# Optimization experiments

Measured on AMD Instinct MI355X. Metric: run time of the kernel, lower is better.

## Reference

```python
import jax, jax.numpy as jnp
import numpy as np

IDIM = 128
ODIM = 128
G = 8          # deformable groups
KH = KW = 3
K = KH * KW


def conv3x3(x, w, b):
    # x: [B,C,H,W], w: [O,I,3,3], stride 1, pad 1
    y = jax.lax.conv_general_dilated(x, w, (1, 1), ((1, 1), (1, 1)),
                                     dimension_numbers=('NCHW', 'OIHW', 'NCHW'))
    return y + b[None, :, None, None]


def deform_conv_v2(x, offset, mask, w, b):
    # x: [B,C,H,W]; offset: [B,2*G*K,H,W]; mask: [B,G*K,H,W] (pre-sigmoid)
    B, C, H, W = x.shape
    Cg = C // G
    off = offset.reshape(B, G, 2 * K, H, W)
    dy = off[:, :, 0::2]            # [B,G,K,H,W]
    dx = off[:, :, 1::2]
    m = jax.nn.sigmoid(mask).reshape(B, G, K, H, W)

    ky, kx = jnp.meshgrid(jnp.arange(KH), jnp.arange(KW), indexing='ij')
    ky = ky.reshape(K).astype(x.dtype)
    kx = kx.reshape(K).astype(x.dtype)
    hh = jnp.arange(H, dtype=x.dtype)
    ww = jnp.arange(W, dtype=x.dtype)
    # sampling positions (stride 1, pad 1, dilation 1)
    py = dy + (ky[:, None, None] + hh[None, :, None] - 1.0)   # [B,G,K,H,W]
    px = dx + (kx[:, None, None] + ww[None, None, :] - 1.0)

    y0 = jnp.floor(py)
    x0 = jnp.floor(px)
    ly = py - y0
    lx = px - x0

    x_flat = x.reshape(B, G, Cg, H * W)

    def gather(yi, xi):
        valid = ((yi >= 0) & (yi < H) & (xi >= 0) & (xi < W)).astype(x.dtype)
        yc = jnp.clip(yi, 0, H - 1).astype(jnp.int32)
        xc = jnp.clip(xi, 0, W - 1).astype(jnp.int32)
        idx = (yc * W + xc).reshape(B, G, 1, K * H * W)
        v = jnp.take_along_axis(x_flat, jnp.broadcast_to(idx, (B, G, Cg, K * H * W)), axis=3)
        return v.reshape(B, G, Cg, K, H, W) * valid[:, :, None]

    # bilinear interpolation with zero padding, fused with modulation mask
    v = (gather(y0, x0) * ((1 - ly) * (1 - lx))[:, :, None]
         + gather(y0, x0 + 1) * ((1 - ly) * lx)[:, :, None]
         + gather(y0 + 1, x0) * (ly * (1 - lx))[:, :, None]
         + gather(y0 + 1, x0 + 1) * (ly * lx)[:, :, None])
    v = v * m[:, :, None]                                      # [B,G,Cg,K,H,W]

    wr = w.reshape(w.shape[0], G, Cg, K)
    out = jnp.einsum('bgckhw,ogck->bohw', v, wr)
    return out + b[None, :, None, None]


def setup_inputs() -> dict:
    key = jax.random.key(0)
    ks = jax.random.split(key, 12)
    B, H, W = 2, 96, 96
    s = 0.05
    return {
        'R1': jax.random.normal(ks[0], (B, IDIM, H, W), jnp.float32),
        'Q0': jax.random.normal(ks[1], (B, IDIM, H, W), jnp.float32),
        'w1': jax.random.normal(ks[2], (ODIM, IDIM, 3, 3), jnp.float32) * s,
        'b1': jax.random.normal(ks[3], (ODIM,), jnp.float32) * s,
        'w2': jax.random.normal(ks[4], (ODIM, ODIM, 3, 3), jnp.float32) * s,
        'b2': jax.random.normal(ks[5], (ODIM,), jnp.float32) * s,
        'w_om': jax.random.normal(ks[6], (G * 3 * K, ODIM, 3, 3), jnp.float32) * s,
        'b_om': jax.random.normal(ks[7], (G * 3 * K,), jnp.float32) * s,
        'w_dcn': jax.random.normal(ks[8], (ODIM, IDIM, 3, 3), jnp.float32) * s,
        'b_dcn': jax.random.normal(ks[9], (ODIM,), jnp.float32) * s,
        'w_rq': jax.random.normal(ks[10], (ODIM, 2 * ODIM, 3, 3), jnp.float32) * s,
        'b_rq': jax.random.normal(ks[11], (ODIM,), jnp.float32) * s,
    }


def reference(R1, Q0, w1, b1, w2, b2, w_om, b_om, w_dcn, b_dcn, w_rq, b_rq):
    off = jax.nn.relu(conv3x3(R1 - Q0, w1, b1))
    off = jax.nn.relu(conv3x3(off, w2, b2))
    om = conv3x3(off, w_om, b_om)                 # [B, 3*G*K, H, W]
    o1, o2, mask = jnp.split(om, 3, axis=1)
    offset = jnp.concatenate([o1, o2], axis=1)    # [B, 2*G*K, H, W]
    fea = jax.nn.relu(deform_conv_v2(R1, offset, mask, w_dcn, b_dcn))
    fused = jnp.concatenate([fea, Q0], axis=1)
    return jax.nn.relu(conv3x3(fused, w_rq, b_rq))
```

## Files before the change

### kernel.cpp

```cpp
#include <hip/hip_runtime.h>

#define HH 96
#define WW 96
#define HW 9216
#define NPIX 18432
#define OMC 216
#define PP 9604

typedef __attribute__((ext_vector_type(8))) short short8x;
typedef __attribute__((ext_vector_type(8))) unsigned short ushort8x;
typedef __attribute__((ext_vector_type(4))) float f32x4;

__device__ __forceinline__ f32x4 mfma16(short8x a, short8x b, f32x4 c) {
    return __builtin_amdgcn_mfma_f32_16x16x32_bf16(a, b, c, 0, 0, 0);
}
__device__ __forceinline__ unsigned short f2bf(float f) {
    unsigned int u = __float_as_uint(f);
    u = (u + 0x7FFFu + ((u >> 16) & 1u)) >> 16;
    return (unsigned short)u;
}
__device__ __forceinline__ float bf2f(unsigned short b) {
    return __uint_as_float((unsigned int)b << 16);
}
__device__ __forceinline__ void split2(float v, unsigned short& h, unsigned short& l) {
    h = f2bf(v);
    l = f2bf(v - bf2f(h));
}
__device__ __forceinline__ void gld_lds16(const unsigned short* src, unsigned short* dst) {
    __builtin_amdgcn_global_load_lds(
        (const __attribute__((address_space(1))) unsigned int*)src,
        (__attribute__((address_space(3))) unsigned int*)dst, 16, 0, 0);
}

__global__ __launch_bounds__(256) void zero_borders(
    unsigned short* __restrict__ diffb,
    unsigned short* __restrict__ t1,
    unsigned short* __restrict__ catb)
{
    int i = blockIdx.x * 256 + threadIdx.x;
    if (i >= 776) return;
    int b = i / 388, r = i % 388;
    int y, x;
    if      (r < 98)  { y = 0;          x = r; }
    else if (r < 196) { y = 97;         x = r - 98; }
    else if (r < 292) { y = r - 196 + 1; x = 0; }
    else              { y = r - 292 + 1; x = 97; }
    size_t P = (size_t)b * PP + (size_t)y * 98 + x;
    ushort8x z = {};
    #pragma unroll
    for (int c = 0; c < 32; ++c) *(ushort8x*)&diffb[P * 256 + c * 8] = z;
    #pragma unroll
    for (int c = 0; c < 32; ++c) *(ushort8x*)&t1[P * 256 + c * 8] = z;
    #pragma unroll
    for (int c = 0; c < 64; ++c) *(ushort8x*)&catb[P * 512 + c * 8] = z;
}

__global__ __launch_bounds__(256) void prep_acts(
    const float* __restrict__ R1, const float* __restrict__ Q0,
    float* __restrict__ r1f,
    unsigned short* __restrict__ diffb,
    unsigned short* __restrict__ cat)
{
    __shared__ float tR[128][64];
    __shared__ float tQ[128][64];
    int tid = threadIdx.x;
    int p0  = blockIdx.x * 64;
    int b   = p0 / HW;
    int rem0 = p0 % HW;

    for (int e = tid; e < 2048; e += 256) {
        int c = e >> 4, j = e & 15;
        size_t base = ((size_t)(b * 128 + c)) * HW + rem0;
        *(float4*)&tR[c][j * 4] = *(const float4*)(R1 + base + j * 4);
        *(float4*)&tQ[c][j * 4] = *(const float4*)(Q0 + base + j * 4);
    }
    __syncthreads();

    int p = tid & 63, half = tid >> 6;
    int c0 = half * 32;
    int pix = p0 + p;
    int rm = pix % HW, yy = rm / 96, xx = rm % 96;
    size_t P = (size_t)b * PP + (size_t)(yy + 1) * 98 + xx + 1;
    float rv[32];
    ushort8x dh[4], dl[4], qh[4], ql[4];
    #pragma unroll
    for (int cc = 0; cc < 32; ++cc) {
        float r = tR[c0 + cc][p], q = tQ[c0 + cc][p];
        rv[cc] = r;
        unsigned short h, l;
        split2(r - q, h, l); dh[cc >> 3][cc & 7] = h; dl[cc >> 3][cc & 7] = l;
        split2(q, h, l);     qh[cc >> 3][cc & 7] = h; ql[cc >> 3][cc & 7] = l;
    }
    #pragma unroll
    for (int i = 0; i < 8; ++i)
        *(float4*)&r1f[(size_t)pix * 128 + c0 + i * 4] = *(float4*)&rv[i * 4];
    #pragma unroll
    for (int i = 0; i < 4; ++i) {
        *(ushort8x*)&diffb[P * 256 +       c0 + i * 8] = dh[i];
        *(ushort8x*)&diffb[P * 256 + 128 + c0 + i * 8] = dl[i];
        *(ushort8x*)&cat [P * 512 + 128 + c0 + i * 8] = qh[i];
        *(ushort8x*)&cat [P * 512 + 384 + c0 + i * 8] = ql[i];
    }
}

__global__ __launch_bounds__(256) void prep_w(
    const float* __restrict__ w1, const float* __restrict__ w2,
    const float* __restrict__ wom, const float* __restrict__ bom,
    const float* __restrict__ wrq, const float* __restrict__ wdcn,
    unsigned short* __restrict__ p1, unsigned short* __restrict__ p2,
    unsigned short* __restrict__ pom, unsigned short* __restrict__ prq,
    unsigned short* __restrict__ pdcn, float* __restrict__ bomp)
{
    int idx = blockIdx.x * 256 + threadIdx.x;
    unsigned short h, l;
    if (idx < 147456) {
        int t = idx / 16384, o = (idx >> 7) & 127, ci = idx & 127;
        int src = (o * 128 + ci) * 9 + t;
        split2(w1[src], h, l);  p1[idx] = h;  p1[idx + 147456] = l;
        split2(w2[src], h, l);  p2[idx] = h;  p2[idx + 147456] = l;
        int dd = o * 1152 + t * 128 + ci;
        split2(wdcn[src], h, l); pdcn[dd] = h; pdcn[dd + 147456] = l;
    }
    if (idx < 294912) {
        {
            int t = idx / 32768, o = (idx >> 7) & 255, ci = idx & 127;
            float v = (o < OMC) ? wom[(o * 128 + ci) * 9 + t] : 0.f;
            split2(v, h, l); pom[idx] = h; pom[idx + 294912] = l;
        }
        {
            int t = idx / 32768, o = (idx >> 8) & 127, ci = idx & 255;
            split2(wrq[(o * 256 + ci) * 9 + t], h, l);
            prq[idx] = h; prq[idx + 294912] = l;
        }
    }
    if (idx < 256) bomp[idx] = (idx < OMC) ? bom[idx] : 0.f;
}

template<int CIN, int COUTP, int MODE, bool RELU>
__global__ __launch_bounds__(256, 2) void conv_mfma(
    const unsigned short* __restrict__ in,
    const unsigned short* __restrict__ wpk,
    const float* __restrict__ bias,
    void* __restrict__ outv)
{
    constexpr int NKC = CIN / 32;
    constexpr int NSTEP = 9 * NKC;
    const size_t WPLANE = (size_t)9 * COUTP * CIN;

    __shared__ __align__(16) unsigned short s_buf[2][3072 + 8192];

    int tid = threadIdx.x;
    int wid = tid >> 6, lane = tid & 63;
    int r = lane & 15, q = lane >> 4;
    int bid = blockIdx.x;
    int swz = (bid & 7) * 48 + (bid >> 3);
    int rowid = swz >> 1, half = swz & 1;
    int b = rowid / 96, y = rowid % 96;
    int x0 = half * 48;
    int nbase = blockIdx.y * 128;

    auto stage = [&](int buf, int step) {
        int t = step / NKC, kc = step - t * NKC;
        int dy = t / 3 - 1, dx = t % 3 - 1;
        unsigned short* sb = &s_buf[buf][0];
        {
            int j = tid;
            int m = j >> 7, pl = (j >> 6) & 1, L = j & 63;
            int px = m * 16 + (L & 15), qd = L >> 4;
            const unsigned short* src = in +
                ((size_t)b * PP + (size_t)(y + 1 + dy) * 98 + (x0 + 1 + dx + px)) * (2 * CIN)
                + pl * CIN + kc * 32 + qd * 8;
            gld_lds16(src, sb + (size_t)(wid * 64) * 8);
        }
        if (tid < 128) {
            int j = 256 + tid;
            int m = j >> 7, pl = (j >> 6) & 1, L = j & 63;
            int px = m * 16 + (L & 15), qd = L >> 4;
            const unsigned short* src = in +
                ((size_t)b * PP + (size_t)(y + 1 + dy) * 98 + (x0 + 1 + dx + px)) * (2 * CIN)
                + pl * CIN + kc * 32 + qd * 8;
            gld_lds16(src, sb + (size_t)(256 + wid * 64) * 8);
        }
        const unsigned short* wbase = wpk + ((size_t)t * COUTP + nbase) * CIN + kc * 32;
        #pragma unroll
        for (int c = 0; c < 4; ++c) {
            int j = c * 256 + tid;
            int ni = (j >> 7) & 1, pl = (j >> 6) & 1, L = j & 63;
            int rr = L & 15, qq = L >> 4;
            const unsigned short* src = wbase + (size_t)pl * WPLANE
                + (size_t)(c * 32 + ni * 16 + rr) * CIN + qq * 8;
            gld_lds16(src, sb + 3072 + (size_t)(c * 256 + wid * 64) * 8);
        }
    };

    f32x4 acc[3][2] = {};

    auto compute = [&](int buf) {
        const unsigned short* sb = &s_buf[buf][0];
        short8x AH[3], AL[3], BH[2], BL[2];
        #pragma unroll
        for (int m = 0; m < 3; ++m) {
            AH[m] = *(const short8x*)(sb + m * 1024 + lane * 8);
            AL[m] = *(const short8x*)(sb + m * 1024 + 512 + lane * 8);
        }
        #pragma unroll
        for (int n = 0; n < 2; ++n) {
            BH[n] = *(const short8x*)(sb + 3072 + wid * 2048 + n * 1024 + lane * 8);
            BL[n] = *(const short8x*)(sb + 3072 + wid * 2048 + n * 1024 + 512 + lane * 8);
        }
        #pragma unroll
        for (int m = 0; m < 3; ++m) {
            #pragma unroll
            for (int n = 0; n < 2; ++n) {
                acc[m][n] = mfma16(AH[m], BH[n], acc[m][n]);
                acc[m][n] = mfma16(AL[m], BH[n], acc[m][n]);
                acc[m][n] = mfma16(AH[m], BL[n], acc[m][n]);
            }
        }
    };

    stage(0, 0);
    __syncthreads();
    int cur = 0;
    for (int k = 0; k < NSTEP; ++k) {
        if (k + 1 < NSTEP) stage(cur ^ 1, k + 1);
        compute(cur);
        __syncthreads();
        cur ^= 1;
    }

    #pragma unroll
    for (int m = 0; m < 3; ++m) {
        #pragma unroll
        for (int n = 0; n < 2; ++n) {
            int o = nbase + wid * 32 + n * 16 + r;
            float bv = bias[o];
            #pragma unroll
            for (int j = 0; j < 4; ++j) {
                int px = m * 16 + q * 4 + j;
                int xx = x0 + px;
                float v = acc[m][n][j] + bv;
                if (RELU) v = fmaxf(v, 0.f);
                if (MODE == 0) {
                    size_t P = (size_t)b * PP + (size_t)(y + 1) * 98 + xx + 1;
                    unsigned short h, l; split2(v, h, l);
                    ((unsigned short*)outv)[P * 2 * COUTP + o] = h;
                    ((unsigned short*)outv)[P * 2 * COUTP + COUTP + o] = l;
                } else if (MODE == 1) {
                    if (o < OMC)
                        ((unsigned short*)outv)[((size_t)b * HW + y * 96 + xx) * OMC + o] = f2bf(v);
                } else {
                    ((float*)outv)[((size_t)b * 128 + o) * HW + y * 96 + xx] = v;
                }
            }
        }
    }
}

__global__ __launch_bounds__(256) void deform_mfma(
    const float* __restrict__ xf,
    const unsigned short* __restrict__ omf,
    const unsigned short* __restrict__ wpk,
    const float* __restrict__ bias,
    unsigned short* __restrict__ cat)
{
    __shared__ __align__(16) unsigned short s_vh[16][1152];
    __shared__ __align__(16) unsigned short s_vl[16][1152];

    int tid = threadIdx.x;
    int pix0 = blockIdx.x * 16;
    int b = pix0 / HW;

    for (int e = tid; e < 1152; e += 256) {
        int p = e / 72, gk = e % 72;
        int pix = pix0 + p;
        int rem = pix % HW;
        int hh = rem / 96, ww = rem % 96;
        int g = gk / 9, k = gk % 9;
        const unsigned short* op = omf + (size_t)pix * OMC;
        float dy = bf2f(op[g * 18 + 2 * k]);
        float dx = bf2f(op[g * 18 + 2 * k + 1]);
        float mr = bf2f(op[144 + g * 9 + k]);
        float m = 1.f / (1.f + __expf(-mr));
        float py = dy + (float)(k / 3) + (float)hh - 1.f;
        float px = dx + (float)(k % 3) + (float)ww - 1.f;
        float fy = floorf(py), fx = floorf(px);
        int y0 = (int)fy, x0 = (int)fx;
        float ly = py - fy, lx = px - fx;
        float cw[4] = {(1.f - ly) * (1.f - lx), (1.f - ly) * lx,
                       ly * (1.f - lx), ly * lx};
        const float* cp[4];
        #pragma unroll
        for (int j = 0; j < 4; ++j) {
            int yy = y0 + (j >> 1), xx = x0 + (j & 1);
            bool valid = (yy >= 0) && (yy < HH) && (xx >= 0) && (xx < WW);
            int yc = yy < 0 ? 0 : (yy > 95 ? 95 : yy);
            int xc = xx < 0 ? 0 : (xx > 95 ? 95 : xx);
            cp[j] = xf + ((size_t)(b * HW + yc * 96 + xc)) * 128 + g * 16;
            cw[j] = valid ? cw[j] * m : 0.f;
        }
        int swz = (p & 7) << 3;
        int i0 = k * 128 + g * 16;
        ushort8x vh[2], vl[2];
        #pragma unroll
        for (int cq = 0; cq < 4; ++cq) {
            float4 v0 = *(const float4*)(cp[0] + cq * 4);
            float4 v1 = *(const float4*)(cp[1] + cq * 4);
            float4 v2 = *(const float4*)(cp[2] + cq * 4);
            float4 v3 = *(const float4*)(cp[3] + cq * 4);
            float vv[4] = {
                cw[0]*v0.x + cw[1]*v1.x + cw[2]*v2.x + cw[3]*v3.x,
                cw[0]*v0.y + cw[1]*v1.y + cw[2]*v2.y + cw[3]*v3.y,
                cw[0]*v0.z + cw[1]*v1.z + cw[2]*v2.z + cw[3]*v3.z,
                cw[0]*v0.w + cw[1]*v1.w + cw[2]*v2.w + cw[3]*v3.w};
            #pragma unroll
            for (int cc = 0; cc < 4; ++cc) {
                unsigned short h, l;
                split2(vv[cc], h, l);
                int ei = cq * 4 + cc;
                vh[ei >> 3][ei & 7] = h;
                vl[ei >> 3][ei & 7] = l;
            }
        }
        *(ushort8x*)&s_vh[p][(i0    ) ^ swz] = vh[0];
        *(ushort8x*)&s_vh[p][(i0 + 8) ^ swz] = vh[1];
        *(ushort8x*)&s_vl[p][(i0    ) ^ swz] = vl[0];
        *(ushort8x*)&s_vl[p][(i0 + 8) ^ swz] = vl[1];
    }
    __syncthreads();

    int wid = tid >> 6, lane = tid & 63;
    int r = lane & 15, q = lane >> 4;
    int n0 = wid * 32;
    f32x4 acc0 = {}, acc1 = {};
    const unsigned short* wb = wpk + (size_t)(n0 + r) * 1152 + q * 8;
    int swz = (r & 7) << 3;
    #pragma unroll
    for (int ch = 0; ch < 9; ++ch) {
        short8x ah[4], al[4], b0h[4], b1h[4], b0l[4], b1l[4];
        #pragma unroll
        for (int k2 = 0; k2 < 4; ++k2) {
            const int kc = ch * 4 + k2;
            int e0 = (kc * 32 + q * 8) ^ swz;
            ah[k2]  = *(const short8x*)&s_vh[r][e0];
            al[k2]  = *(const short8x*)&s_vl[r][e0];
            b0h[k2] = *(const short8x*)(wb + kc * 32);
            b1h[k2] = *(const short8x*)(wb + (size_t)16 * 1152 + kc * 32);
            b0l[k2] = *(const short8x*)(wb + 147456 + kc * 32);
            b1l[k2] = *(const short8x*)(wb + 147456 + (size_t)16 * 1152 + kc * 32);
        }
        #pragma unroll
        for (int k2 = 0; k2 < 4; ++k2) {
            acc0 = mfma16(ah[k2], b0h[k2], acc0);
            acc1 = mfma16(ah[k2], b1h[k2], acc1);
            acc0 = mfma16(al[k2], b0h[k2], acc0);
            acc1 = mfma16(al[k2], b1h[k2], acc1);
            acc0 = mfma16(ah[k2], b0l[k2], acc0);
            acc1 = mfma16(ah[k2], b1l[k2], acc1);
        }
    }
    #pragma unroll
    for (int ni = 0; ni < 2; ++ni) {
        f32x4 A = ni ? acc1 : acc0;
        int o = n0 + ni * 16 + r;
        float bv = bias[o];
        #pragma unroll
        for (int j = 0; j < 4; ++j) {
            int pixel = pix0 + q * 4 + j;
            int bb = pixel / HW, rm = pixel % HW;
            int yy = rm / 96, xx = rm % 96;
            size_t P = (size_t)bb * PP + (size_t)(yy + 1) * 98 + xx + 1;
            float v = fmaxf(A[j] + bv, 0.f);
            unsigned short h, l;
            split2(v, h, l);
            cat[P * 512 + o] = h;
            cat[P * 512 + 256 + o] = l;
        }
    }
}

extern "C" void kernel_launch(void* const* d_in, const int* in_sizes, int n_in,
                              void* d_out, int out_size, void* d_ws, size_t ws_size,
                              hipStream_t stream) {
    const float* R1    = (const float*)d_in[0];
    const float* Q0    = (const float*)d_in[1];
    const float* w1    = (const float*)d_in[2];
    const float* b1    = (const float*)d_in[3];
    const float* w2    = (const float*)d_in[4];
    const float* b2    = (const float*)d_in[5];
    const float* w_om  = (const float*)d_in[6];
    const float* b_om  = (const float*)d_in[7];
    const float* w_dcn = (const float*)d_in[8];
    const float* b_dcn = (const float*)d_in[9];
    const float* w_rq  = (const float*)d_in[10];
    const float* b_rq  = (const float*)d_in[11];
    float* outp = (float*)d_out;

    char* w = (char*)d_ws;
    float*          r1f   = (float*)w;          w += (size_t)NPIX * 128 * 4;
    unsigned short* diffb = (unsigned short*)w; w += (size_t)2 * PP * 256 * 2;
    unsigned short* t1    = (unsigned short*)w; w += (size_t)2 * PP * 256 * 2;
    unsigned short* catb  = (unsigned short*)w; w += (size_t)2 * PP * 512 * 2;
    unsigned short* p1    = (unsigned short*)w; w += 2 * 147456 * 2;
    unsigned short* p2    = (unsigned short*)w; w += 2 * 147456 * 2;
    unsigned short* pdcn  = (unsigned short*)w; w += 2 * 147456 * 2;
    unsigned short* pom   = (unsigned short*)w; w += 2 * 294912 * 2;
    unsigned short* prq   = (unsigned short*)w; w += 2 * 294912 * 2;
    float*          bomp  = (float*)w;          w += 256 * 4;
    unsigned short* t2    = diffb;
    unsigned short* omf   = t1;

    zero_borders<<<4, 256, 0, stream>>>(diffb, t1, catb);
    prep_acts<<<288, 256, 0, stream>>>(R1, Q0, r1f, diffb, catb);
    prep_w<<<1152, 256, 0, stream>>>(w1, w2, w_om, b_om, w_rq, w_dcn,
                                     p1, p2, pom, prq, pdcn, bomp);

    conv_mfma<128, 128, 0, true ><<<dim3(384, 1), 256, 0, stream>>>(diffb, p1, b1, t1);
    conv_mfma<128, 128, 0, true ><<<dim3(384, 1), 256, 0, stream>>>(t1,    p2, b2, t2);
    conv_mfma<128, 256, 1, false><<<dim3(384, 2), 256, 0, stream>>>(t2,   pom, bomp, omf);

    deform_mfma<<<1152, 256, 0, stream>>>(r1f, omf, pdcn, b_dcn, catb);

    conv_mfma<256, 128, 2, true ><<<dim3(384, 1), 256, 0, stream>>>(catb, prq, b_rq, outp);
}
```

Baseline: 432.4 us.

## Gather deformable samples from bf16 input and drop low-part split in deform GEMM

R1 is now stored as single bf16 instead of fp32 for the deformable gather, which halves the gather traffic. Sampled values are written to shared memory as one bf16 array rather than a hi/lo split, so the deform GEMM does 4 MFMAs per k-chunk instead of 6. The DCN weight packing is reordered to match a (group, tap, channel) column order so the shared-memory tile can be written contiguously without a swizzle, and launch bounds now request 4 blocks per CU. The cost is lower precision in the deformable-conv input and activations, with possible LDS bank conflicts now that the swizzle is gone.

```diff
diff --git a/kernel.cpp b/kernel.cpp
--- a/kernel.cpp
+++ b/kernel.cpp
@@ -57,7 +57,7 @@
 
 __global__ __launch_bounds__(256) void prep_acts(
     const float* __restrict__ R1, const float* __restrict__ Q0,
-    float* __restrict__ r1f,
+    unsigned short* __restrict__ r1b,
     unsigned short* __restrict__ diffb,
     unsigned short* __restrict__ cat)
 {
@@ -81,21 +81,18 @@
     int pix = p0 + p;
     int rm = pix % HW, yy = rm / 96, xx = rm % 96;
     size_t P = (size_t)b * PP + (size_t)(yy + 1) * 98 + xx + 1;
-    float rv[32];
-    ushort8x dh[4], dl[4], qh[4], ql[4];
+    ushort8x rb[4], dh[4], dl[4], qh[4], ql[4];
     #pragma unroll
     for (int cc = 0; cc < 32; ++cc) {
         float r = tR[c0 + cc][p], q = tQ[c0 + cc][p];
-        rv[cc] = r;
+        rb[cc >> 3][cc & 7] = f2bf(r);
         unsigned short h, l;
         split2(r - q, h, l); dh[cc >> 3][cc & 7] = h; dl[cc >> 3][cc & 7] = l;
         split2(q, h, l);     qh[cc >> 3][cc & 7] = h; ql[cc >> 3][cc & 7] = l;
     }
     #pragma unroll
-    for (int i = 0; i < 8; ++i)
-        *(float4*)&r1f[(size_t)pix * 128 + c0 + i * 4] = *(float4*)&rv[i * 4];
-    #pragma unroll
     for (int i = 0; i < 4; ++i) {
+        *(ushort8x*)&r1b[(size_t)pix * 128 + c0 + i * 8] = rb[i];
         *(ushort8x*)&diffb[P * 256 +       c0 + i * 8] = dh[i];
         *(ushort8x*)&diffb[P * 256 + 128 + c0 + i * 8] = dl[i];
         *(ushort8x*)&cat [P * 512 + 128 + c0 + i * 8] = qh[i];
@@ -118,7 +115,7 @@
         int src = (o * 128 + ci) * 9 + t;
         split2(w1[src], h, l);  p1[idx] = h;  p1[idx + 147456] = l;
         split2(w2[src], h, l);  p2[idx] = h;  p2[idx + 147456] = l;
-        int dd = o * 1152 + t * 128 + ci;
+        int dd = o * 1152 + ((ci >> 4) * 9 + t) * 16 + (ci & 15);
         split2(wdcn[src], h, l); pdcn[dd] = h; pdcn[dd + 147456] = l;
     }
     if (idx < 294912) {
@@ -257,22 +254,21 @@
     }
 }
 
-__global__ __launch_bounds__(256) void deform_mfma(
-    const float* __restrict__ xf,
+__global__ __launch_bounds__(256, 4) void deform_mfma(
+    const unsigned short* __restrict__ xb,
     const unsigned short* __restrict__ omf,
     const unsigned short* __restrict__ wpk,
     const float* __restrict__ bias,
     unsigned short* __restrict__ cat)
 {
-    __shared__ __align__(16) unsigned short s_vh[16][1152];
-    __shared__ __align__(16) unsigned short s_vl[16][1152];
+    __shared__ __align__(16) unsigned short s_v[16][1160];
 
     int tid = threadIdx.x;
     int pix0 = blockIdx.x * 16;
     int b = pix0 / HW;
 
     for (int e = tid; e < 1152; e += 256) {
-        int p = e / 72, gk = e % 72;
+        int p = e & 15, gk = e >> 4;
         int pix = pix0 + p;
         int rem = pix % HW;
         int hh = rem / 96, ww = rem % 96;
@@ -289,43 +285,31 @@
         float ly = py - fy, lx = px - fx;
         float cw[4] = {(1.f - ly) * (1.f - lx), (1.f - ly) * lx,
                        ly * (1.f - lx), ly * lx};
-        const float* cp[4];
+        ushort8x cv0[4], cv1[4];
         #pragma unroll
         for (int j = 0; j < 4; ++j) {
             int yy = y0 + (j >> 1), xx = x0 + (j & 1);
             bool valid = (yy >= 0) && (yy < HH) && (xx >= 0) && (xx < WW);
             int yc = yy < 0 ? 0 : (yy > 95 ? 95 : yy);
             int xc = xx < 0 ? 0 : (xx > 95 ? 95 : xx);
-            cp[j] = xf + ((size_t)(b * HW + yc * 96 + xc)) * 128 + g * 16;
+            const unsigned short* cp =
+                xb + ((size_t)(b * HW + yc * 96 + xc)) * 128 + g * 16;
+            cv0[j] = *(const ushort8x*)cp;
+            cv1[j] = *(const ushort8x*)(cp + 8);
             cw[j] = valid ? cw[j] * m : 0.f;
         }
-        int swz = (p & 7) << 3;
-        int i0 = k * 128 + g * 16;
-        ushort8x vh[2], vl[2];
-        #pragma unroll
-        for (int cq = 0; cq < 4; ++cq) {
-            float4 v0 = *(const float4*)(cp[0] + cq * 4);
-            float4 v1 = *(const float4*)(cp[1] + cq * 4);
-            float4 v2 = *(const float4*)(cp[2] + cq * 4);
-            float4 v3 = *(const float4*)(cp[3] + cq * 4);
-            float vv[4] = {
-                cw[0]*v0.x + cw[1]*v1.x + cw[2]*v2.x + cw[3]*v3.x,
-                cw[0]*v0.y + cw[1]*v1.y + cw[2]*v2.y + cw[3]*v3.y,
-                cw[0]*v0.z + cw[1]*v1.z + cw[2]*v2.z + cw[3]*v3.z,
-                cw[0]*v0.w + cw[1]*v1.w + cw[2]*v2.w + cw[3]*v3.w};
-            #pragma unroll
-            for (int cc = 0; cc < 4; ++cc) {
-                unsigned short h, l;
-                split2(vv[cc], h, l);
-                int ei = cq * 4 + cc;
-                vh[ei >> 3][ei & 7] = h;
-                vl[ei >> 3][ei & 7] = l;
-            }
-        }
-        *(ushort8x*)&s_vh[p][(i0    ) ^ swz] = vh[0];
-        *(ushort8x*)&s_vh[p][(i0 + 8) ^ swz] = vh[1];
-        *(ushort8x*)&s_vl[p][(i0    ) ^ swz] = vl[0];
-        *(ushort8x*)&s_vl[p][(i0 + 8) ^ swz] = vl[1];
+        ushort8x o0, o1;
+        #pragma unroll
+        for (int i = 0; i < 8; ++i) {
+            float v0 = cw[0] * bf2f(cv0[0][i]) + cw[1] * bf2f(cv0[1][i])
+                     + cw[2] * bf2f(cv0[2][i]) + cw[3] * bf2f(cv0[3][i]);
+            float v1 = cw[0] * bf2f(cv1[0][i]) + cw[1] * bf2f(cv1[1][i])
+                     + cw[2] * bf2f(cv1[2][i]) + cw[3] * bf2f(cv1[3][i]);
+            o0[i] = f2bf(v0);
+            o1[i] = f2bf(v1);
+        }
+        *(ushort8x*)&s_v[p][gk * 16    ] = o0;
+        *(ushort8x*)&s_v[p][gk * 16 + 8] = o1;
     }
     __syncthreads();
 
@@ -334,30 +318,27 @@
     int n0 = wid * 32;
     f32x4 acc0 = {}, acc1 = {};
     const unsigned short* wb = wpk + (size_t)(n0 + r) * 1152 + q * 8;
-    int swz = (r & 7) << 3;
-    #pragma unroll
-    for (int ch = 0; ch < 9; ++ch) {
-        short8x ah[4], al[4], b0h[4], b1h[4], b0l[4], b1l[4];
-        #pragma unroll
-        for (int k2 = 0; k2 < 4; ++k2) {
-            const int kc = ch * 4 + k2;
-            int e0 = (kc * 32 + q * 8) ^ swz;
-            ah[k2]  = *(const short8x*)&s_vh[r][e0];
-            al[k2]  = *(const short8x*)&s_vl[r][e0];
-            b0h[k2] = *(const short8x*)(wb + kc * 32);
-            b1h[k2] = *(const short8x*)(wb + (size_t)16 * 1152 + kc * 32);
-            b0l[k2] = *(const short8x*)(wb + 147456 + kc * 32);
-            b1l[k2] = *(const short8x*)(wb + 147456 + (size_t)16 * 1152 + kc * 32);
-        }
-        #pragma unroll
-        for (int k2 = 0; k2 < 4; ++k2) {
-            acc0 = mfma16(ah[k2], b0h[k2], acc0);
-            acc1 = mfma16(ah[k2], b1h[k2], acc1);
-            acc0 = mfma16(al[k2], b0h[k2], acc0);
-            acc1 = mfma16(al[k2], b1h[k2], acc1);
-            acc0 = mfma16(ah[k2], b0l[k2], acc0);
-            acc1 = mfma16(ah[k2], b1l[k2], acc1);
-        }
+    #pragma unroll
+    for (int kp = 0; kp < 18; ++kp) {
+        const int k0 = kp * 2, k1 = k0 + 1;
+        short8x a0 = *(const short8x*)&s_v[r][k0 * 32 + q * 8];
+        short8x a1 = *(const short8x*)&s_v[r][k1 * 32 + q * 8];
+        short8x w00 = *(const short8x*)(wb + k0 * 32);
+        short8x w10 = *(const short8x*)(wb + (size_t)16 * 1152 + k0 * 32);
+        short8x l00 = *(const short8x*)(wb + 147456 + k0 * 32);
+        short8x l10 = *(const short8x*)(wb + 147456 + (size_t)16 * 1152 + k0 * 32);
+        short8x w01 = *(const short8x*)(wb + k1 * 32);
+        short8x w11 = *(const short8x*)(wb + (size_t)16 * 1152 + k1 * 32);
+        short8x l01 = *(const short8x*)(wb + 147456 + k1 * 32);
+        short8x l11 = *(const short8x*)(wb + 147456 + (size_t)16 * 1152 + k1 * 32);
+        acc0 = mfma16(a0, w00, acc0);
+        acc1 = mfma16(a0, w10, acc1);
+        acc0 = mfma16(a0, l00, acc0);
+        acc1 = mfma16(a0, l10, acc1);
+        acc0 = mfma16(a1, w01, acc0);
+        acc1 = mfma16(a1, w11, acc1);
+        acc0 = mfma16(a1, l01, acc0);
+        acc1 = mfma16(a1, l11, acc1);
     }
     #pragma unroll
     for (int ni = 0; ni < 2; ++ni) {
@@ -397,7 +378,7 @@
     float* outp = (float*)d_out;
 
     char* w = (char*)d_ws;
-    float*          r1f   = (float*)w;          w += (size_t)NPIX * 128 * 4;
+    unsigned short* r1b   = (unsigned short*)w; w += (size_t)NPIX * 128 * 2;
     unsigned short* diffb = (unsigned short*)w; w += (size_t)2 * PP * 256 * 2;
     unsigned short* t1    = (unsigned short*)w; w += (size_t)2 * PP * 256 * 2;
     unsigned short* catb  = (unsigned short*)w; w += (size_t)2 * PP * 512 * 2;
@@ -411,7 +392,7 @@
     unsigned short* omf   = t1;
 
     zero_borders<<<4, 256, 0, stream>>>(diffb, t1, catb);
-    prep_acts<<<288, 256, 0, stream>>>(R1, Q0, r1f, diffb, catb);
+    prep_acts<<<288, 256, 0, stream>>>(R1, Q0, r1b, diffb, catb);
     prep_w<<<1152, 256, 0, stream>>>(w1, w2, w_om, b_om, w_rq, w_dcn,
                                      p1, p2, pom, prq, pdcn, bomp);
 
@@ -419,7 +400,7 @@
     conv_mfma<128, 128, 0, true ><<<dim3(384, 1), 256, 0, stream>>>(t1,    p2, b2, t2);
     conv_mfma<128, 256, 1, false><<<dim3(384, 2), 256, 0, stream>>>(t2,   pom, bomp, omf);
 
-    deform_mfma<<<1152, 256, 0, stream>>>(r1f, omf, pdcn, b_dcn, catb);
+    deform_mfma<<<1152, 256, 0, stream>>>(r1b, omf, pdcn, b_dcn, catb);
 
     conv_mfma<256, 128, 2, true ><<<dim3(384, 1), 256, 0, stream>>>(catb, prq, b_rq, outp);
 }
```

New measurement: 413.1 us. 4.5% less time.
